# Kernel optimization log

Hardware: AMD Instinct MI355X
Metric: run time of the kernel (lower is better)

Reference implementation:

```python
import jax, jax.numpy as jnp
import numpy as np

B = 32768          # batch rows
IN_DIM = 512
HID = 64           # hidden_dim fixed in module
COMM = 128         # output_dim == proto_latent_dim (num_simultaneous_tokens=1)
P = 2048           # num_protos
BETA = 0.25        # settings.alpha != 0
KL_W = 1.0         # settings.kl_weight
ENT_W = 0.1        # settings.entropy_weight
EPSILON = 1e-8


def setup_inputs() -> dict:
    key = jax.random.key(0)
    ks = jax.random.split(key, 16)
    s = 0.05
    return {
        "x": jax.random.normal(ks[0], (B, IN_DIM), jnp.float32),
        "eps": jax.random.normal(ks[1], (B, COMM), jnp.float32),
        "W_emb": jax.random.normal(ks[2], (IN_DIM, HID), jnp.float32) * s,
        "b_emb": jnp.zeros((HID,), jnp.float32),
        "W1": jax.random.normal(ks[3], (HID, HID), jnp.float32) * s,
        "b1": jnp.zeros((HID,), jnp.float32),
        "W2": jax.random.normal(ks[4], (HID, COMM), jnp.float32) * s,
        "b2": jnp.zeros((COMM,), jnp.float32),
        "W_mu": jax.random.normal(ks[5], (COMM, COMM), jnp.float32) * s,
        "b_mu": jnp.zeros((COMM,), jnp.float32),
        "W_var": jax.random.normal(ks[6], (COMM, COMM), jnp.float32) * s,
        "b_var": jnp.zeros((COMM,), jnp.float32),
        "protos": jax.random.uniform(ks[7], (P, COMM), jnp.float32, -1.0 / P, 1.0 / P),
    }


def _sq_dists(a, b):
    # ||a||^2 + ||b||^2 - 2 a b^T  -> [N, P] without [N,P,D] intermediate
    return (jnp.sum(a * a, axis=1, keepdims=True)
            + jnp.sum(b * b, axis=1)
            - 2.0 * a @ b.T)


def reference(x, eps, W_emb, b_emb, W1, b1, W2, b2, W_mu, b_mu, W_var, b_var, protos):
    sg = jax.lax.stop_gradient
    h = x @ W_emb + b_emb                       # [B, HID]
    h = h.reshape(-1, HID)                      # num_imgs = 1
    h = jax.nn.relu(h @ W1 + b1)
    h = jax.nn.relu(h @ W2 + b2)                # [B, COMM]
    r = h.reshape(-1, COMM)
    mu = r @ W_mu + b_mu
    logvar = r @ W_var + b_var
    sample = mu + jnp.exp(0.5 * logvar) * eps   # reparameterize

    # VQ: pairwise squared dists, argmin routing, codebook gather
    dists = _sq_dists(sample, protos)           # [B, P]
    idx = jnp.argmin(dists, axis=1)             # [B]
    quantized = protos[idx]                     # [B, COMM]

    commitment_loss = jnp.mean((sg(quantized) - mu) ** 2)
    embedding_loss = jnp.mean((quantized - sg(mu)) ** 2)
    vq_loss = BETA * commitment_loss + embedding_loss

    # entropy term: softmax-like row probs from Gaussian kernel on mu-proto dists
    # sum(((mu-p)/2)^2, -1) == ||mu-p||^2 / 4, computed via matmul form
    neg_dist = -0.5 * (_sq_dists(mu, protos) / 4.0)
    exponents = jnp.exp(neg_dist) + EPSILON     # [B, P]
    row_probs = exponents / jnp.sum(exponents, axis=1, keepdims=True)
    approx_probs = jnp.mean(row_probs, axis=0)  # [P]
    ent = jnp.sum(-approx_probs * jnp.log(approx_probs))
    vq_loss = vq_loss + ENT_W * ent

    # straight-through estimator
    q_st = sample + sg(quantized - sample)
    output = q_st.reshape(-1, COMM)

    kld = jnp.mean(-0.5 * jnp.sum(1.0 + logvar - mu ** 2 - jnp.exp(logvar), axis=1))
    total_loss = KL_W * kld + vq_loss
    return output, total_loss, kld
```

## Files before the change

kernel.cpp:

```cpp
#include <hip/hip_runtime.h>
#include <cmath>

constexpr int NB   = 32768;
constexpr int IND  = 512;
constexpr int HIDD = 64;
constexpr int CM   = 128;
constexpr int NP   = 2048;
constexpr float BETA  = 0.25f;
constexpr float ENT_W = 0.1f;
constexpr float EPSV  = 1e-8f;

typedef __attribute__((ext_vector_type(8))) short short8v;
typedef __attribute__((ext_vector_type(4))) float f32x4v;

__device__ __forceinline__ float4 ld4(const float* p){ return *reinterpret_cast<const float4*>(p); }
__device__ __forceinline__ void  st4(float* p, float4 v){ *reinterpret_cast<float4*>(p) = v; }

__device__ __forceinline__ unsigned short f2bf(float f){
  union { float f; unsigned u; } v; v.f = f;
  unsigned r = v.u + 0x7fffu + ((v.u >> 16) & 1u);
  return (unsigned short)(r >> 16);
}
__device__ __forceinline__ float bf2f(unsigned short u){
  union { unsigned u; float f; } v; v.u = ((unsigned)u) << 16;
  return v.f;
}
__device__ __forceinline__ short8v cvt8(float4 a, float4 b){
  short8v r;
  r[0]=(short)f2bf(a.x); r[1]=(short)f2bf(a.y); r[2]=(short)f2bf(a.z); r[3]=(short)f2bf(a.w);
  r[4]=(short)f2bf(b.x); r[5]=(short)f2bf(b.y); r[6]=(short)f2bf(b.z); r[7]=(short)f2bf(b.w);
  return r;
}

__device__ __forceinline__ float wave_sum(float v){
  #pragma unroll
  for (int m = 1; m < 64; m <<= 1) v += __shfl_xor(v, m, 64);
  return v;
}

typedef __attribute__((address_space(1))) unsigned int gu32;
typedef __attribute__((address_space(3))) unsigned int su32;
__device__ __forceinline__ void gload_lds16(const void* g, void* s){
  __builtin_amdgcn_global_load_lds((const gu32*)g, (su32*)s, 16, 0, 0);
}
__device__ __forceinline__ void gload_lds4(const void* g, void* s){
  __builtin_amdgcn_global_load_lds((const gu32*)g, (su32*)s, 4, 0, 0);
}
__device__ __forceinline__ void barrier_raw(){
  __builtin_amdgcn_sched_barrier(0);
  __builtin_amdgcn_s_barrier();
  __builtin_amdgcn_sched_barrier(0);
}

__global__ __launch_bounds__(256) void k_prep(const float* __restrict__ protos,
                                              float* __restrict__ normp2,
                                              unsigned short* __restrict__ pBF,
                                              const float* __restrict__ W_emb,
                                              const float* __restrict__ W1,
                                              const float* __restrict__ W2,
                                              const float* __restrict__ Wmu,
                                              const float* __restrict__ Wvar,
                                              unsigned short* __restrict__ WembT,
                                              unsigned short* __restrict__ W1T,
                                              unsigned short* __restrict__ W2T,
                                              unsigned short* __restrict__ WmuT,
                                              unsigned short* __restrict__ WvarT){
  const int b = blockIdx.x, tid = threadIdx.x;
  if (b < 8){
    const int p = b * 256 + tid;
    const float* row = protos + (size_t)p * CM;
    float s = 0.f;
    #pragma unroll
    for (int k = 0; k < CM; k += 4){
      float4 v = ld4(row + k);
      s += v.x*v.x + v.y*v.y + v.z*v.z + v.w*v.w;
      ushort4 u; u.x = f2bf(v.x); u.y = f2bf(v.y); u.z = f2bf(v.z); u.w = f2bf(v.w);
      *reinterpret_cast<ushort4*>(&pBF[(size_t)p * CM + k]) = u;
    }
    normp2[p] = s;
  } else if (b < 16){
    const int nb = (b - 8) * 8;
    for (int i = tid; i < 8*512; i += 256){
      const int n = nb + (i >> 9), k = i & 511;
      WembT[n*512 + k] = f2bf(W_emb[k*64 + n]);
    }
  } else if (b == 16){
    for (int i = tid; i < 64*64; i += 256){
      const int n = i >> 6, k = i & 63;
      W1T[n*64 + k] = f2bf(W1[k*64 + n]);
    }
  } else if (b == 17){
    for (int i = tid; i < 128*64; i += 256){
      const int n = i >> 6, k = i & 63;
      W2T[n*64 + k] = f2bf(W2[k*128 + n]);
    }
  } else if (b < 20){
    const int nb = (b - 18) * 64;
    for (int i = tid; i < 64*128; i += 256){
      const int n = nb + (i >> 7), k = i & 127;
      WmuT[n*128 + k] = f2bf(Wmu[k*128 + n]);
    }
  } else {
    const int nb = (b - 20) * 64;
    for (int i = tid; i < 64*128; i += 256){
      const int n = nb + (i >> 7), k = i & 127;
      WvarT[n*128 + k] = f2bf(Wvar[k*128 + n]);
    }
  }
}

__global__ __launch_bounds__(256, 4) void fwd_fused(const float* __restrict__ x,
    const unsigned short* __restrict__ WembT, const float* __restrict__ b_emb,
    const unsigned short* __restrict__ W1T,   const float* __restrict__ b1,
    const unsigned short* __restrict__ W2T,   const float* __restrict__ b2,
    const unsigned short* __restrict__ WmuT,  const float* __restrict__ bmu,
    const unsigned short* __restrict__ WvarT, const float* __restrict__ bvar,
    const float* __restrict__ epsIn,
    unsigned short* __restrict__ muBF, unsigned short* __restrict__ sBF,
    float* __restrict__ normMu2, float* __restrict__ kld_part){
  __shared__ __align__(16) unsigned short SH[16384];
  __shared__ __align__(16) unsigned short Xs[4096];
  unsigned short* h1s = SH;
  unsigned short* h2s = SH + 4096;
  unsigned short* h3s = SH + 8192;
  unsigned short* muS = SH;
  unsigned short* sS  = SH + 8192;
  __shared__ float redbuf[4];

  const int tid = threadIdx.x;
  const int w = tid >> 6, l = tid & 63;
  const int lr = l >> 4, lc = l & 15;
  const int rowbase = blockIdx.x * 64;
  const int row = w*16 + lc;

  f32x4v acc1[4];
  #pragma unroll
  for (int nt = 0; nt < 4; nt++) acc1[nt] = (f32x4v){0.f,0.f,0.f,0.f};
  const int srow = tid >> 2, sq = tid & 3;
  const float* xrow = x + (size_t)(rowbase + srow) * IND + sq*16;
  for (int kc8 = 0; kc8 < 8; kc8++){
    float4 v0 = ld4(xrow + kc8*64);
    float4 v1 = ld4(xrow + kc8*64 + 4);
    float4 v2 = ld4(xrow + kc8*64 + 8);
    float4 v3 = ld4(xrow + kc8*64 + 12);
    __syncthreads();
    const int b0 = (srow*64 + sq*16)     ^ ((srow & 7) << 3);
    const int b1i = (srow*64 + sq*16 + 8) ^ ((srow & 7) << 3);
    *reinterpret_cast<short8v*>(&Xs[b0])  = cvt8(v0, v1);
    *reinterpret_cast<short8v*>(&Xs[b1i]) = cvt8(v2, v3);
    __syncthreads();
    #pragma unroll
    for (int ks = 0; ks < 2; ks++){
      const int ai = (row*64 + ks*32 + lr*8) ^ ((row & 7) << 3);
      short8v af = *reinterpret_cast<const short8v*>(&Xs[ai]);
      #pragma unroll
      for (int nt = 0; nt < 4; nt++){
        const int n = nt*16 + lc;
        short8v bf = *reinterpret_cast<const short8v*>(&WembT[(size_t)n*512 + kc8*64 + ks*32 + lr*8]);
        acc1[nt] = __builtin_amdgcn_mfma_f32_16x16x32_bf16(af, bf, acc1[nt], 0, 0, 0);
      }
    }
  }
  #pragma unroll
  for (int nt = 0; nt < 4; nt++){
    const int col = nt*16 + lc;
    const float bb = b_emb[col];
    #pragma unroll
    for (int r = 0; r < 4; r++){
      const int row2 = w*16 + lr*4 + r;
      h1s[(row2*64 + col) ^ ((row2 & 7) << 3)] = f2bf(acc1[nt][r] + bb);
    }
  }
  __syncthreads();

  f32x4v acc2[4];
  #pragma unroll
  for (int nt = 0; nt < 4; nt++) acc2[nt] = (f32x4v){0.f,0.f,0.f,0.f};
  #pragma unroll
  for (int ks = 0; ks < 2; ks++){
    const int ai = (row*64 + ks*32 + lr*8) ^ ((row & 7) << 3);
    short8v af = *reinterpret_cast<const short8v*>(&h1s[ai]);
    #pragma unroll
    for (int nt = 0; nt < 4; nt++){
      const int n = nt*16 + lc;
      short8v bf = *reinterpret_cast<const short8v*>(&W1T[(size_t)n*64 + ks*32 + lr*8]);
      acc2[nt] = __builtin_amdgcn_mfma_f32_16x16x32_bf16(af, bf, acc2[nt], 0, 0, 0);
    }
  }
  __syncthreads();
  #pragma unroll
  for (int nt = 0; nt < 4; nt++){
    const int col = nt*16 + lc;
    const float bb = b1[col];
    #pragma unroll
    for (int r = 0; r < 4; r++){
      const int row2 = w*16 + lr*4 + r;
      h2s[(row2*64 + col) ^ ((row2 & 7) << 3)] = f2bf(fmaxf(acc2[nt][r] + bb, 0.f));
    }
  }
  __syncthreads();

  f32x4v acc3[8];
  #pragma unroll
  for (int nt = 0; nt < 8; nt++) acc3[nt] = (f32x4v){0.f,0.f,0.f,0.f};
  #pragma unroll
  for (int ks = 0; ks < 2; ks++){
    const int ai = (row*64 + ks*32 + lr*8) ^ ((row & 7) << 3);
    short8v af = *reinterpret_cast<const short8v*>(&h2s[ai]);
    #pragma unroll
    for (int nt = 0; nt < 8; nt++){
      const int n = nt*16 + lc;
      short8v bf = *reinterpret_cast<const short8v*>(&W2T[(size_t)n*64 + ks*32 + lr*8]);
      acc3[nt] = __builtin_amdgcn_mfma_f32_16x16x32_bf16(af, bf, acc3[nt], 0, 0, 0);
    }
  }
  #pragma unroll
  for (int nt = 0; nt < 8; nt++){
    const int col = nt*16 + lc;
    const float bb = b2[col];
    #pragma unroll
    for (int r = 0; r < 4; r++){
      const int row2 = w*16 + lr*4 + r;
      h3s[(row2*128 + col) ^ ((row2 & 7) << 3)] = f2bf(fmaxf(acc3[nt][r] + bb, 0.f));
    }
  }
  __syncthreads();

  f32x4v accM[8], accV[8];
  #pragma unroll
  for (int nt = 0; nt < 8; nt++){ accM[nt] = (f32x4v){0.f,0.f,0.f,0.f}; accV[nt] = (f32x4v){0.f,0.f,0.f,0.f}; }
  #pragma unroll
  for (int ks = 0; ks < 4; ks++){
    const int ai = (row*128 + ks*32 + lr*8) ^ ((row & 7) << 3);
    short8v af = *reinterpret_cast<const short8v*>(&h3s[ai]);
    #pragma unroll
    for (int nt = 0; nt < 8; nt++){
      const int n = nt*16 + lc;
      short8v bM = *reinterpret_cast<const short8v*>(&WmuT [(size_t)n*128 + ks*32 + lr*8]);
      short8v bV = *reinterpret_cast<const short8v*>(&WvarT[(size_t)n*128 + ks*32 + lr*8]);
      accM[nt] = __builtin_amdgcn_mfma_f32_16x16x32_bf16(af, bM, accM[nt], 0, 0, 0);
      accV[nt] = __builtin_amdgcn_mfma_f32_16x16x32_bf16(af, bV, accV[nt], 0, 0, 0);
    }
  }
  __syncthreads();

  float kl = 0.f;
  float m2[4] = {0.f, 0.f, 0.f, 0.f};
  #pragma unroll
  for (int nt = 0; nt < 8; nt++){
    const int col = nt*16 + lc;
    const float bm = bmu[col], bv = bvar[col];
    #pragma unroll
    for (int r = 0; r < 4; r++){
      const int row2 = w*16 + lr*4 + r;
      const float mu = accM[nt][r] + bm;
      const float lv = accV[nt][r] + bv;
      const float s2 = __expf(0.5f * lv);
      const float sa = mu + s2 * epsIn[(size_t)(rowbase + row2)*CM + col];
      kl += 1.f + lv - mu*mu - s2*s2;
      m2[r] += mu*mu;
      const int li = (row2*128 + col) ^ ((row2 & 7) << 3);
      muS[li] = f2bf(mu);
      sS [li] = f2bf(sa);
    }
  }
  #pragma unroll
  for (int m = 1; m < 16; m <<= 1){
    #pragma unroll
    for (int r = 0; r < 4; r++) m2[r] += __shfl_xor(m2[r], m, 64);
  }
  if (lc == 0){
    #pragma unroll
    for (int r = 0; r < 4; r++) normMu2[rowbase + w*16 + lr*4 + r] = m2[r];
  }
  const float kw = wave_sum(kl);
  if (l == 0) redbuf[w] = kw;
  __syncthreads();
  if (tid == 0) kld_part[blockIdx.x] = redbuf[0]+redbuf[1]+redbuf[2]+redbuf[3];
  {
    const int r2 = tid >> 2, kq = tid & 3;
    #pragma unroll
    for (int i = 0; i < 4; i++){
      const int k = kq*32 + i*8;
      const int li = (r2*128 + k) ^ ((r2 & 7) << 3);
      short8v vm = *reinterpret_cast<const short8v*>(&muS[li]);
      short8v vs = *reinterpret_cast<const short8v*>(&sS[li]);
      *reinterpret_cast<short8v*>(&muBF[(size_t)(rowbase + r2)*CM + k]) = vm;
      *reinterpret_cast<short8v*>(&sBF [(size_t)(rowbase + r2)*CM + k]) = vs;
    }
  }
}

__global__ __launch_bounds__(512, 4) void proto_merged(
    const unsigned short* __restrict__ sBF, const unsigned short* __restrict__ mBF,
    const unsigned short* __restrict__ pBF, const float* __restrict__ normp2,
    const float* __restrict__ normMu2, const float* __restrict__ protosF,
    float* __restrict__ outA, float* __restrict__ approx_part,
    float* __restrict__ commit_part)
{
  __shared__ __align__(16) unsigned short Ps[3][64*CM];
  __shared__ float Pn[3][64];
  __shared__ float approxl[NP];
  __shared__ float bw[2][64];
  __shared__ int   iw[2][64];
  __shared__ float sw[2][64];
  __shared__ float srow_s[64];
  __shared__ int   bidx_s[64];
  __shared__ float redbuf[8];

  const int tid = threadIdx.x;
  const int w = tid >> 6, l = tid & 63;
  const int lr = l >> 4, lc = l & 15;
  const int rw = w & 1;
  const int pw = (w >> 1) & 1;
  const int mat = w >> 2;
  const int rowbase = blockIdx.x * 64;

  for (int t = tid; t < NP; t += 512) approxl[t] = 0.f;

  const unsigned short* Abase = mat ? mBF : sBF;
  short8v af[2][4];
  #pragma unroll
  for (int mt = 0; mt < 2; mt++){
    const size_t rg = (size_t)(rowbase + rw*32 + mt*16 + lc) * CM;
    #pragma unroll
    for (int ks = 0; ks < 4; ks++)
      af[mt][ks] = *reinterpret_cast<const short8v*>(&Abase[rg + ks*32 + lr*8]);
  }
  float nmn[8];
  #pragma unroll
  for (int mt = 0; mt < 2; mt++)
    #pragma unroll
    for (int r = 0; r < 4; r++)
      nmn[mt*4+r] = -0.125f * normMu2[rowbase + rw*32 + mt*16 + lr*4 + r];

  #define STAGE(pc, buf) {                                                        \
    _Pragma("unroll")                                                             \
    for (int j = 0; j < 2; j++){                                                  \
      const int p = w*8 + j*4 + (l >> 4);                                         \
      const int g = l & 15;                                                       \
      gload_lds16(&pBF[(size_t)((pc) + p)*CM + ((g*8) ^ ((p & 7)*8))],            \
                  &Ps[buf][(w*8 + j*4)*CM]);                                      \
    }                                                                             \
    if (w == 0) gload_lds4(&normp2[(pc) + l], &Pn[buf][0]);                       \
  }
  #define VWAIT_PEND() { if (w == 0) asm volatile("s_waitcnt vmcnt(3)" ::: "memory"); \
                         else        asm volatile("s_waitcnt vmcnt(2)" ::: "memory"); }
  #define VWAIT_ALL()  asm volatile("s_waitcnt vmcnt(0)" ::: "memory")

  float best[8]; int bidx[8]; float sr[8];
  #pragma unroll
  for (int i = 0; i < 8; i++){ best[i] = 3.4e38f; bidx[i] = 0; sr[i] = 0.f; }

  STAGE(0, 0);
  int cur = 0;
  for (int c = 0; c < 32; c++){
    const int nxt = (cur == 2) ? 0 : cur + 1;
    if (c < 31){ STAGE((c+1)*64, nxt); VWAIT_PEND(); }
    else       { VWAIT_ALL(); }
    barrier_raw();
    const float npv0 = Pn[cur][pw*32 + lc];
    const float npv1 = Pn[cur][pw*32 + 16 + lc];
    f32x4v acc[2][2];
    #pragma unroll
    for (int mt = 0; mt < 2; mt++)
      #pragma unroll
      for (int nt = 0; nt < 2; nt++) acc[mt][nt] = (f32x4v){0.f,0.f,0.f,0.f};
    #pragma unroll
    for (int ks = 0; ks < 4; ks++){
      const int pl0 = pw*32 + lc;
      const int pl1 = pw*32 + 16 + lc;
      short8v pf0 = *reinterpret_cast<const short8v*>(&Ps[cur][(pl0*CM + ks*32 + lr*8) ^ ((pl0 & 7) << 3)]);
      short8v pf1 = *reinterpret_cast<const short8v*>(&Ps[cur][(pl1*CM + ks*32 + lr*8) ^ ((pl1 & 7) << 3)]);
      #pragma unroll
      for (int mt = 0; mt < 2; mt++){
        acc[mt][0] = __builtin_amdgcn_mfma_f32_16x16x32_bf16(af[mt][ks], pf0, acc[mt][0], 0, 0, 0);
        acc[mt][1] = __builtin_amdgcn_mfma_f32_16x16x32_bf16(af[mt][ks], pf1, acc[mt][1], 0, 0, 0);
      }
    }
    const int pc = c*64;
    if (mat == 0){
      #pragma unroll
      for (int nt = 0; nt < 2; nt++){
        const int pg = pc + pw*32 + nt*16 + lc;
        const float npv = nt ? npv1 : npv0;
        #pragma unroll
        for (int mt = 0; mt < 2; mt++)
          #pragma unroll
          for (int r = 0; r < 4; r++){
            const float sc = fmaf(-2.f, acc[mt][nt][r], npv);
            if (sc < best[mt*4+r]){ best[mt*4+r] = sc; bidx[mt*4+r] = pg; }
          }
      }
    } else {
      #pragma unroll
      for (int nt = 0; nt < 2; nt++){
        const float pvn = -0.125f * (nt ? npv1 : npv0);
        #pragma unroll
        for (int mt = 0; mt < 2; mt++)
          #pragma unroll
          for (int r = 0; r < 4; r++)
            sr[mt*4+r] += __expf(fmaf(0.25f, acc[mt][nt][r], nmn[mt*4+r] + pvn));
      }
    }
    cur = nxt;
  }

  if (mat == 0){
    #pragma unroll
    for (int m = 1; m < 16; m <<= 1){
      #pragma unroll
      for (int i = 0; i < 8; i++){
        const float ob = __shfl_xor(best[i], m, 64);
        const int   oi = __shfl_xor(bidx[i], m, 64);
        if (ob < best[i] || (ob == best[i] && oi < bidx[i])){ best[i] = ob; bidx[i] = oi; }
      }
    }
    if (lc == 0){
      #pragma unroll
      for (int mt = 0; mt < 2; mt++)
        #pragma unroll
        for (int r = 0; r < 4; r++){
          const int row = rw*32 + mt*16 + lr*4 + r;
          bw[pw][row] = best[mt*4+r];
          iw[pw][row] = bidx[mt*4+r];
        }
    }
  } else {
    #pragma unroll
    for (int m = 1; m < 16; m <<= 1){
      #pragma unroll
      for (int i = 0; i < 8; i++) sr[i] += __shfl_xor(sr[i], m, 64);
    }
    if (lc == 0){
      #pragma unroll
      for (int mt = 0; mt < 2; mt++)
        #pragma unroll
        for (int r = 0; r < 4; r++){
          const int row = rw*32 + mt*16 + lr*4 + r;
          sw[pw][row] = sr[mt*4+r];
        }
    }
  }
  __syncthreads();
  if (tid < 64){
    float b0 = bw[0][tid]; int i0 = iw[0][tid];
    const float b1 = bw[1][tid]; const int i1 = iw[1][tid];
    if (b1 < b0 || (b1 == b0 && i1 < i0)){ b0 = b1; i0 = i1; }
    bidx_s[tid] = i0;
    srow_s[tid] = sw[0][tid] + sw[1][tid] + (float)NP * EPSV;
  }
  STAGE(0, 0);
  __syncthreads();

  {
    const int row = tid >> 3, cp = tid & 7;
    const int rowg = rowbase + row;
    const int idx = bidx_s[row];
    float cl = 0.f;
    #pragma unroll
    for (int c4 = 0; c4 < 4; c4++){
      const int cc = c4*32 + cp*4;
      float4 q = ld4(protosF + (size_t)idx * CM + cc);
      ushort4 mb = *reinterpret_cast<const ushort4*>(&mBF[(size_t)rowg * CM + cc]);
      st4(outA + (size_t)rowg * CM + cc, q);
      const float dx=q.x-bf2f(mb.x), dy=q.y-bf2f(mb.y), dz=q.z-bf2f(mb.z), dw=q.w-bf2f(mb.w);
      cl += dx*dx + dy*dy + dz*dz + dw*dw;
    }
    const float cw = wave_sum(cl);
    if (l == 0) redbuf[w] = cw;
  }
  float rs[8]; float epsc = 0.f;
  #pragma unroll
  for (int mt = 0; mt < 2; mt++)
    #pragma unroll
    for (int r = 0; r < 4; r++){
      rs[mt*4+r] = 1.0f / srow_s[rw*32 + mt*16 + lr*4 + r];
      epsc += rs[mt*4+r];
    }
  epsc *= EPSV;
  if (mat == 0){
    #pragma unroll
    for (int mt = 0; mt < 2; mt++){
      const size_t rg = (size_t)(rowbase + rw*32 + mt*16 + lc) * CM;
      #pragma unroll
      for (int ks = 0; ks < 4; ks++)
        af[mt][ks] = *reinterpret_cast<const short8v*>(&mBF[rg + ks*32 + lr*8]);
    }
  }
  __syncthreads();
  if (tid == 0) commit_part[blockIdx.x] = redbuf[0]+redbuf[1]+redbuf[2]+redbuf[3]
                                        + redbuf[4]+redbuf[5]+redbuf[6]+redbuf[7];

  const int pq = w >> 1;
  cur = 0;
  for (int c = 0; c < 32; c++){
    const int nxt = (cur == 2) ? 0 : cur + 1;
    if (c < 31){ STAGE((c+1)*64, nxt); VWAIT_PEND(); }
    else       { VWAIT_ALL(); }
    barrier_raw();
    const int pl = pq*16 + lc;
    const float npv = Pn[cur][pl];
    f32x4v accB[2];
    accB[0] = (f32x4v){0.f,0.f,0.f,0.f};
    accB[1] = (f32x4v){0.f,0.f,0.f,0.f};
    #pragma unroll
    for (int ks = 0; ks < 4; ks++){
      short8v pf = *reinterpret_cast<const short8v*>(&Ps[cur][(pl*CM + ks*32 + lr*8) ^ ((pl & 7) << 3)]);
      accB[0] = __builtin_amdgcn_mfma_f32_16x16x32_bf16(af[0][ks], pf, accB[0], 0, 0, 0);
      accB[1] = __builtin_amdgcn_mfma_f32_16x16x32_bf16(af[1][ks], pf, accB[1], 0, 0, 0);
    }
    const float pvn = -0.125f * npv;
    float cs = epsc;
    #pragma unroll
    for (int mt = 0; mt < 2; mt++)
      #pragma unroll
      for (int r = 0; r < 4; r++){
        const float e = __expf(fmaf(0.25f, accB[mt][r], nmn[mt*4+r] + pvn));
        cs = fmaf(e, rs[mt*4+r], cs);
      }
    cs += __shfl_xor(cs, 16, 64);
    cs += __shfl_xor(cs, 32, 64);
    if (l < 16) atomicAdd(&approxl[c*64 + pq*16 + lc], cs);
    cur = nxt;
  }
  __syncthreads();
  for (int t = tid; t < NP; t += 512)
    approx_part[(size_t)blockIdx.x * NP + t] = approxl[t];
  #undef STAGE
  #undef VWAIT_PEND
  #undef VWAIT_ALL
}

__global__ __launch_bounds__(256) void k4a(const float* __restrict__ approx_part,
                                           float* __restrict__ ent_part){
  __shared__ float red[128];
  const int tid = threadIdx.x;
  const int p = blockIdx.x * 32 + (tid & 31);
  const int slice = tid >> 5;
  float s = 0.f;
  for (int b = slice; b < 512; b += 8) s += approx_part[(size_t)b * NP + p];
  s += __shfl_xor(s, 32, 64);
  if ((tid & 63) < 32) red[(tid >> 6)*32 + (tid & 31)] = s;
  __syncthreads();
  if (tid < 32){
    const float a = (red[tid] + red[32+tid] + red[64+tid] + red[96+tid]) * (1.0f / 32768.0f);
    float t = -a * logf(a);
    #pragma unroll
    for (int m = 1; m < 32; m <<= 1) t += __shfl_xor(t, m, 32);
    if (tid == 0) ent_part[blockIdx.x] = t;
  }
}

__global__ __launch_bounds__(256) void k4b(const float* __restrict__ kld_part,
                                           const float* __restrict__ commit_part,
                                           const float* __restrict__ ent_part,
                                           float* __restrict__ outs){
  __shared__ float redbuf[8];
  const int tid = threadIdx.x;
  float k = 0.f, c = 0.f;
  for (int i = tid; i < 512; i += 256){ k += kld_part[i]; c += commit_part[i]; }
  float kw = wave_sum(k), cw = wave_sum(c);
  if ((tid & 63) == 0){ redbuf[tid >> 6] = kw; redbuf[4 + (tid >> 6)] = cw; }
  __syncthreads();
  if (tid == 0){
    float ks = redbuf[0] + redbuf[1] + redbuf[2] + redbuf[3];
    float cs = redbuf[4] + redbuf[5] + redbuf[6] + redbuf[7];
    float es = 0.f;
    for (int i = 0; i < 64; i++) es += ent_part[i];
    float kld = -0.5f * ks / 32768.0f;
    float m = cs / (32768.0f * 128.0f);
    float vq = BETA * m + m + ENT_W * es;
    outs[0] = kld + vq;
    outs[1] = kld;
  }
}

extern "C" void kernel_launch(void* const* d_in, const int* in_sizes, int n_in,
                              void* d_out, int out_size, void* d_ws, size_t ws_size,
                              hipStream_t stream){
  const float* x      = (const float*)d_in[0];
  const float* epsIn  = (const float*)d_in[1];
  const float* W_emb  = (const float*)d_in[2];
  const float* b_emb  = (const float*)d_in[3];
  const float* W1     = (const float*)d_in[4];
  const float* b1     = (const float*)d_in[5];
  const float* W2     = (const float*)d_in[6];
  const float* b2     = (const float*)d_in[7];
  const float* W_mu   = (const float*)d_in[8];
  const float* b_mu   = (const float*)d_in[9];
  const float* W_var  = (const float*)d_in[10];
  const float* b_var  = (const float*)d_in[11];
  const float* protos = (const float*)d_in[12];
  float* out = (float*)d_out;
  float* ws = (float*)d_ws;

  const size_t M1 = 1024u * 1024u;
  unsigned short* mBF  = (unsigned short*)ws;
  unsigned short* sBF  = (unsigned short*)(ws + 2*M1);
  float* approx_part = ws + 4*M1;
  float* tail = ws + 5*M1;
  float* normMu2     = tail;
  float* normp2      = normMu2 + 32768;
  float* kld_part    = normp2 + 2048;
  float* commit_part = kld_part + 512;
  float* ent_part    = commit_part + 512;
  unsigned short* pBF   = (unsigned short*)(ent_part + 64);
  unsigned short* WembT = pBF + (size_t)NP*CM;
  unsigned short* W1T   = WembT + 64*512;
  unsigned short* W2T   = W1T + 64*64;
  unsigned short* WmuT  = W2T + 128*64;
  unsigned short* WvarT = WmuT + 128*128;

  k_prep<<<22, 256, 0, stream>>>(protos, normp2, pBF, W_emb, W1, W2, W_mu, W_var,
                                 WembT, W1T, W2T, WmuT, WvarT);
  fwd_fused<<<NB/64, 256, 0, stream>>>(x, WembT, b_emb, W1T, b1, W2T, b2,
                                       WmuT, b_mu, WvarT, b_var, epsIn,
                                       mBF, sBF, normMu2, kld_part);
  proto_merged<<<NB/64, 512, 0, stream>>>(sBF, mBF, pBF, normp2, normMu2,
                                          protos, out, approx_part, commit_part);
  k4a<<<64, 256, 0, stream>>>(approx_part, ent_part);
  k4b<<<1, 256, 0, stream>>>(kld_part, commit_part, ent_part, out + (size_t)NB * CM);
}
```

Baseline: 165.7 us.

## Fuse MLP encoder kernel into proto distance kernel, keep mu/sample in LDS

Merges the encoder MLP kernel and the prototype distance/argmin/entropy kernel into a single 512-thread kernel. mu and sample stay in shared memory as bf16 instead of round-tripping through global memory, and the first prototype tile is staged before the KL epilogue so its load overlaps that work. The MLP work is now split across 8 waves, each covering half the output columns. LDS is repartitioned into one aliased buffer, which raises shared-memory use per block and may reduce occupancy.

```diff
diff --git a/kernel.cpp b/kernel.cpp
--- a/kernel.cpp
+++ b/kernel.cpp
@@ -109,198 +109,21 @@
   }
 }
 
-__global__ __launch_bounds__(256, 4) void fwd_fused(const float* __restrict__ x,
+__global__ __launch_bounds__(512, 4) void mega(const float* __restrict__ x,
     const unsigned short* __restrict__ WembT, const float* __restrict__ b_emb,
     const unsigned short* __restrict__ W1T,   const float* __restrict__ b1,
     const unsigned short* __restrict__ W2T,   const float* __restrict__ b2,
     const unsigned short* __restrict__ WmuT,  const float* __restrict__ bmu,
     const unsigned short* __restrict__ WvarT, const float* __restrict__ bvar,
     const float* __restrict__ epsIn,
-    unsigned short* __restrict__ muBF, unsigned short* __restrict__ sBF,
-    float* __restrict__ normMu2, float* __restrict__ kld_part){
-  __shared__ __align__(16) unsigned short SH[16384];
-  __shared__ __align__(16) unsigned short Xs[4096];
-  unsigned short* h1s = SH;
-  unsigned short* h2s = SH + 4096;
-  unsigned short* h3s = SH + 8192;
-  unsigned short* muS = SH;
-  unsigned short* sS  = SH + 8192;
-  __shared__ float redbuf[4];
-
-  const int tid = threadIdx.x;
-  const int w = tid >> 6, l = tid & 63;
-  const int lr = l >> 4, lc = l & 15;
-  const int rowbase = blockIdx.x * 64;
-  const int row = w*16 + lc;
-
-  f32x4v acc1[4];
-  #pragma unroll
-  for (int nt = 0; nt < 4; nt++) acc1[nt] = (f32x4v){0.f,0.f,0.f,0.f};
-  const int srow = tid >> 2, sq = tid & 3;
-  const float* xrow = x + (size_t)(rowbase + srow) * IND + sq*16;
-  for (int kc8 = 0; kc8 < 8; kc8++){
-    float4 v0 = ld4(xrow + kc8*64);
-    float4 v1 = ld4(xrow + kc8*64 + 4);
-    float4 v2 = ld4(xrow + kc8*64 + 8);
-    float4 v3 = ld4(xrow + kc8*64 + 12);
-    __syncthreads();
-    const int b0 = (srow*64 + sq*16)     ^ ((srow & 7) << 3);
-    const int b1i = (srow*64 + sq*16 + 8) ^ ((srow & 7) << 3);
-    *reinterpret_cast<short8v*>(&Xs[b0])  = cvt8(v0, v1);
-    *reinterpret_cast<short8v*>(&Xs[b1i]) = cvt8(v2, v3);
-    __syncthreads();
-    #pragma unroll
-    for (int ks = 0; ks < 2; ks++){
-      const int ai = (row*64 + ks*32 + lr*8) ^ ((row & 7) << 3);
-      short8v af = *reinterpret_cast<const short8v*>(&Xs[ai]);
-      #pragma unroll
-      for (int nt = 0; nt < 4; nt++){
-        const int n = nt*16 + lc;
-        short8v bf = *reinterpret_cast<const short8v*>(&WembT[(size_t)n*512 + kc8*64 + ks*32 + lr*8]);
-        acc1[nt] = __builtin_amdgcn_mfma_f32_16x16x32_bf16(af, bf, acc1[nt], 0, 0, 0);
-      }
-    }
-  }
-  #pragma unroll
-  for (int nt = 0; nt < 4; nt++){
-    const int col = nt*16 + lc;
-    const float bb = b_emb[col];
-    #pragma unroll
-    for (int r = 0; r < 4; r++){
-      const int row2 = w*16 + lr*4 + r;
-      h1s[(row2*64 + col) ^ ((row2 & 7) << 3)] = f2bf(acc1[nt][r] + bb);
-    }
-  }
-  __syncthreads();
-
-  f32x4v acc2[4];
-  #pragma unroll
-  for (int nt = 0; nt < 4; nt++) acc2[nt] = (f32x4v){0.f,0.f,0.f,0.f};
-  #pragma unroll
-  for (int ks = 0; ks < 2; ks++){
-    const int ai = (row*64 + ks*32 + lr*8) ^ ((row & 7) << 3);
-    short8v af = *reinterpret_cast<const short8v*>(&h1s[ai]);
-    #pragma unroll
-    for (int nt = 0; nt < 4; nt++){
-      const int n = nt*16 + lc;
-      short8v bf = *reinterpret_cast<const short8v*>(&W1T[(size_t)n*64 + ks*32 + lr*8]);
-      acc2[nt] = __builtin_amdgcn_mfma_f32_16x16x32_bf16(af, bf, acc2[nt], 0, 0, 0);
-    }
-  }
-  __syncthreads();
-  #pragma unroll
-  for (int nt = 0; nt < 4; nt++){
-    const int col = nt*16 + lc;
-    const float bb = b1[col];
-    #pragma unroll
-    for (int r = 0; r < 4; r++){
-      const int row2 = w*16 + lr*4 + r;
-      h2s[(row2*64 + col) ^ ((row2 & 7) << 3)] = f2bf(fmaxf(acc2[nt][r] + bb, 0.f));
-    }
-  }
-  __syncthreads();
-
-  f32x4v acc3[8];
-  #pragma unroll
-  for (int nt = 0; nt < 8; nt++) acc3[nt] = (f32x4v){0.f,0.f,0.f,0.f};
-  #pragma unroll
-  for (int ks = 0; ks < 2; ks++){
-    const int ai = (row*64 + ks*32 + lr*8) ^ ((row & 7) << 3);
-    short8v af = *reinterpret_cast<const short8v*>(&h2s[ai]);
-    #pragma unroll
-    for (int nt = 0; nt < 8; nt++){
-      const int n = nt*16 + lc;
-      short8v bf = *reinterpret_cast<const short8v*>(&W2T[(size_t)n*64 + ks*32 + lr*8]);
-      acc3[nt] = __builtin_amdgcn_mfma_f32_16x16x32_bf16(af, bf, acc3[nt], 0, 0, 0);
-    }
-  }
-  #pragma unroll
-  for (int nt = 0; nt < 8; nt++){
-    const int col = nt*16 + lc;
-    const float bb = b2[col];
-    #pragma unroll
-    for (int r = 0; r < 4; r++){
-      const int row2 = w*16 + lr*4 + r;
-      h3s[(row2*128 + col) ^ ((row2 & 7) << 3)] = f2bf(fmaxf(acc3[nt][r] + bb, 0.f));
-    }
-  }
-  __syncthreads();
-
-  f32x4v accM[8], accV[8];
-  #pragma unroll
-  for (int nt = 0; nt < 8; nt++){ accM[nt] = (f32x4v){0.f,0.f,0.f,0.f}; accV[nt] = (f32x4v){0.f,0.f,0.f,0.f}; }
-  #pragma unroll
-  for (int ks = 0; ks < 4; ks++){
-    const int ai = (row*128 + ks*32 + lr*8) ^ ((row & 7) << 3);
-    short8v af = *reinterpret_cast<const short8v*>(&h3s[ai]);
-    #pragma unroll
-    for (int nt = 0; nt < 8; nt++){
-      const int n = nt*16 + lc;
-      short8v bM = *reinterpret_cast<const short8v*>(&WmuT [(size_t)n*128 + ks*32 + lr*8]);
-      short8v bV = *reinterpret_cast<const short8v*>(&WvarT[(size_t)n*128 + ks*32 + lr*8]);
-      accM[nt] = __builtin_amdgcn_mfma_f32_16x16x32_bf16(af, bM, accM[nt], 0, 0, 0);
-      accV[nt] = __builtin_amdgcn_mfma_f32_16x16x32_bf16(af, bV, accV[nt], 0, 0, 0);
-    }
-  }
-  __syncthreads();
-
-  float kl = 0.f;
-  float m2[4] = {0.f, 0.f, 0.f, 0.f};
-  #pragma unroll
-  for (int nt = 0; nt < 8; nt++){
-    const int col = nt*16 + lc;
-    const float bm = bmu[col], bv = bvar[col];
-    #pragma unroll
-    for (int r = 0; r < 4; r++){
-      const int row2 = w*16 + lr*4 + r;
-      const float mu = accM[nt][r] + bm;
-      const float lv = accV[nt][r] + bv;
-      const float s2 = __expf(0.5f * lv);
-      const float sa = mu + s2 * epsIn[(size_t)(rowbase + row2)*CM + col];
-      kl += 1.f + lv - mu*mu - s2*s2;
-      m2[r] += mu*mu;
-      const int li = (row2*128 + col) ^ ((row2 & 7) << 3);
-      muS[li] = f2bf(mu);
-      sS [li] = f2bf(sa);
-    }
-  }
-  #pragma unroll
-  for (int m = 1; m < 16; m <<= 1){
-    #pragma unroll
-    for (int r = 0; r < 4; r++) m2[r] += __shfl_xor(m2[r], m, 64);
-  }
-  if (lc == 0){
-    #pragma unroll
-    for (int r = 0; r < 4; r++) normMu2[rowbase + w*16 + lr*4 + r] = m2[r];
-  }
-  const float kw = wave_sum(kl);
-  if (l == 0) redbuf[w] = kw;
-  __syncthreads();
-  if (tid == 0) kld_part[blockIdx.x] = redbuf[0]+redbuf[1]+redbuf[2]+redbuf[3];
-  {
-    const int r2 = tid >> 2, kq = tid & 3;
-    #pragma unroll
-    for (int i = 0; i < 4; i++){
-      const int k = kq*32 + i*8;
-      const int li = (r2*128 + k) ^ ((r2 & 7) << 3);
-      short8v vm = *reinterpret_cast<const short8v*>(&muS[li]);
-      short8v vs = *reinterpret_cast<const short8v*>(&sS[li]);
-      *reinterpret_cast<short8v*>(&muBF[(size_t)(rowbase + r2)*CM + k]) = vm;
-      *reinterpret_cast<short8v*>(&sBF [(size_t)(rowbase + r2)*CM + k]) = vs;
-    }
-  }
-}
-
-__global__ __launch_bounds__(512, 4) void proto_merged(
-    const unsigned short* __restrict__ sBF, const unsigned short* __restrict__ mBF,
     const unsigned short* __restrict__ pBF, const float* __restrict__ normp2,
-    const float* __restrict__ normMu2, const float* __restrict__ protosF,
+    const float* __restrict__ protosF,
     float* __restrict__ outA, float* __restrict__ approx_part,
-    float* __restrict__ commit_part)
+    float* __restrict__ commit_part, float* __restrict__ kld_part)
 {
-  __shared__ __align__(16) unsigned short Ps[3][64*CM];
+  __shared__ __align__(16) unsigned short SH[36864];
   __shared__ float Pn[3][64];
-  __shared__ float approxl[NP];
+  __shared__ float nm2_s[2][64];
   __shared__ float bw[2][64];
   __shared__ int   iw[2][64];
   __shared__ float sw[2][64];
@@ -308,31 +131,128 @@
   __shared__ int   bidx_s[64];
   __shared__ float redbuf[8];
 
+  unsigned short* muS = SH;
+  float* approxl      = (float*)(SH + 8192);
+  unsigned short* PsU = SH + 12288;
+  unsigned short* Xs  = PsU;
+  unsigned short* h1s = PsU + 4096;
+  unsigned short* h2s = PsU + 8192;
+  unsigned short* h3s = PsU + 12288;
+  unsigned short* sS  = PsU + 16384;
+
   const int tid = threadIdx.x;
   const int w = tid >> 6, l = tid & 63;
   const int lr = l >> 4, lc = l & 15;
-  const int rw = w & 1;
-  const int pw = (w >> 1) & 1;
-  const int mat = w >> 2;
   const int rowbase = blockIdx.x * 64;
 
-  for (int t = tid; t < NP; t += 512) approxl[t] = 0.f;
-
-  const unsigned short* Abase = mat ? mBF : sBF;
-  short8v af[2][4];
-  #pragma unroll
-  for (int mt = 0; mt < 2; mt++){
-    const size_t rg = (size_t)(rowbase + rw*32 + mt*16 + lc) * CM;
-    #pragma unroll
-    for (int ks = 0; ks < 4; ks++)
-      af[mt][ks] = *reinterpret_cast<const short8v*>(&Abase[rg + ks*32 + lr*8]);
-  }
-  float nmn[8];
-  #pragma unroll
-  for (int mt = 0; mt < 2; mt++)
-    #pragma unroll
-    for (int r = 0; r < 4; r++)
-      nmn[mt*4+r] = -0.125f * normMu2[rowbase + rw*32 + mt*16 + lr*4 + r];
+  const int rq = w & 3, nh = w >> 2;
+  const int row = rq*16 + lc;
+
+  f32x4v acc1[2];
+  acc1[0] = (f32x4v){0.f,0.f,0.f,0.f}; acc1[1] = (f32x4v){0.f,0.f,0.f,0.f};
+  const int srow = tid >> 3, sq = tid & 7;
+  const float* xrow = x + (size_t)(rowbase + srow) * IND + sq*8;
+  for (int kc8 = 0; kc8 < 8; kc8++){
+    float4 v0 = ld4(xrow + kc8*64);
+    float4 v1 = ld4(xrow + kc8*64 + 4);
+    __syncthreads();
+    *reinterpret_cast<short8v*>(&Xs[(srow*64 + sq*8) ^ ((srow & 7) << 3)]) = cvt8(v0, v1);
+    __syncthreads();
+    #pragma unroll
+    for (int ks = 0; ks < 2; ks++){
+      const int ai = (row*64 + ks*32 + lr*8) ^ ((row & 7) << 3);
+      short8v af = *reinterpret_cast<const short8v*>(&Xs[ai]);
+      #pragma unroll
+      for (int nt = 0; nt < 2; nt++){
+        const int n = nh*32 + nt*16 + lc;
+        short8v bf = *reinterpret_cast<const short8v*>(&WembT[(size_t)n*512 + kc8*64 + ks*32 + lr*8]);
+        acc1[nt] = __builtin_amdgcn_mfma_f32_16x16x32_bf16(af, bf, acc1[nt], 0, 0, 0);
+      }
+    }
+  }
+  __syncthreads();
+  #pragma unroll
+  for (int nt = 0; nt < 2; nt++){
+    const int col = nh*32 + nt*16 + lc;
+    const float bb = b_emb[col];
+    #pragma unroll
+    for (int r = 0; r < 4; r++){
+      const int row2 = rq*16 + lr*4 + r;
+      h1s[(row2*64 + col) ^ ((row2 & 7) << 3)] = f2bf(acc1[nt][r] + bb);
+    }
+  }
+  __syncthreads();
+
+  f32x4v acc2[2];
+  acc2[0] = (f32x4v){0.f,0.f,0.f,0.f}; acc2[1] = (f32x4v){0.f,0.f,0.f,0.f};
+  #pragma unroll
+  for (int ks = 0; ks < 2; ks++){
+    const int ai = (row*64 + ks*32 + lr*8) ^ ((row & 7) << 3);
+    short8v af = *reinterpret_cast<const short8v*>(&h1s[ai]);
+    #pragma unroll
+    for (int nt = 0; nt < 2; nt++){
+      const int n = nh*32 + nt*16 + lc;
+      short8v bf = *reinterpret_cast<const short8v*>(&W1T[(size_t)n*64 + ks*32 + lr*8]);
+      acc2[nt] = __builtin_amdgcn_mfma_f32_16x16x32_bf16(af, bf, acc2[nt], 0, 0, 0);
+    }
+  }
+  __syncthreads();
+  #pragma unroll
+  for (int nt = 0; nt < 2; nt++){
+    const int col = nh*32 + nt*16 + lc;
+    const float bb = b1[col];
+    #pragma unroll
+    for (int r = 0; r < 4; r++){
+      const int row2 = rq*16 + lr*4 + r;
+      h2s[(row2*64 + col) ^ ((row2 & 7) << 3)] = f2bf(fmaxf(acc2[nt][r] + bb, 0.f));
+    }
+  }
+  __syncthreads();
+
+  f32x4v acc3[4];
+  #pragma unroll
+  for (int nt = 0; nt < 4; nt++) acc3[nt] = (f32x4v){0.f,0.f,0.f,0.f};
+  #pragma unroll
+  for (int ks = 0; ks < 2; ks++){
+    const int ai = (row*64 + ks*32 + lr*8) ^ ((row & 7) << 3);
+    short8v af = *reinterpret_cast<const short8v*>(&h2s[ai]);
+    #pragma unroll
+    for (int nt = 0; nt < 4; nt++){
+      const int n = nh*64 + nt*16 + lc;
+      short8v bf = *reinterpret_cast<const short8v*>(&W2T[(size_t)n*64 + ks*32 + lr*8]);
+      acc3[nt] = __builtin_amdgcn_mfma_f32_16x16x32_bf16(af, bf, acc3[nt], 0, 0, 0);
+    }
+  }
+  __syncthreads();
+  #pragma unroll
+  for (int nt = 0; nt < 4; nt++){
+    const int col = nh*64 + nt*16 + lc;
+    const float bb = b2[col];
+    #pragma unroll
+    for (int r = 0; r < 4; r++){
+      const int row2 = rq*16 + lr*4 + r;
+      h3s[(row2*128 + col) ^ ((row2 & 7) << 3)] = f2bf(fmaxf(acc3[nt][r] + bb, 0.f));
+    }
+  }
+  __syncthreads();
+
+  f32x4v accM[4], accV[4];
+  #pragma unroll
+  for (int nt = 0; nt < 4; nt++){ accM[nt] = (f32x4v){0.f,0.f,0.f,0.f}; accV[nt] = (f32x4v){0.f,0.f,0.f,0.f}; }
+  #pragma unroll
+  for (int ks = 0; ks < 4; ks++){
+    const int ai = (row*128 + ks*32 + lr*8) ^ ((row & 7) << 3);
+    short8v af = *reinterpret_cast<const short8v*>(&h3s[ai]);
+    #pragma unroll
+    for (int nt = 0; nt < 4; nt++){
+      const int n = nh*64 + nt*16 + lc;
+      short8v bM = *reinterpret_cast<const short8v*>(&WmuT [(size_t)n*128 + ks*32 + lr*8]);
+      short8v bV = *reinterpret_cast<const short8v*>(&WvarT[(size_t)n*128 + ks*32 + lr*8]);
+      accM[nt] = __builtin_amdgcn_mfma_f32_16x16x32_bf16(af, bM, accM[nt], 0, 0, 0);
+      accV[nt] = __builtin_amdgcn_mfma_f32_16x16x32_bf16(af, bV, accV[nt], 0, 0, 0);
+    }
+  }
+  __syncthreads();
 
   #define STAGE(pc, buf) {                                                        \
     _Pragma("unroll")                                                             \
@@ -340,7 +260,7 @@
       const int p = w*8 + j*4 + (l >> 4);                                         \
       const int g = l & 15;                                                       \
       gload_lds16(&pBF[(size_t)((pc) + p)*CM + ((g*8) ^ ((p & 7)*8))],            \
-                  &Ps[buf][(w*8 + j*4)*CM]);                                      \
+                  &PsU[(size_t)(buf)*8192 + (w*8 + j*4)*CM]);                     \
     }                                                                             \
     if (w == 0) gload_lds4(&normp2[(pc) + l], &Pn[buf][0]);                       \
   }
@@ -348,11 +268,73 @@
                          else        asm volatile("s_waitcnt vmcnt(2)" ::: "memory"); }
   #define VWAIT_ALL()  asm volatile("s_waitcnt vmcnt(0)" ::: "memory")
 
+  STAGE(0, 0);
+
+  {
+    float kl = 0.f;
+    float m2[4] = {0.f, 0.f, 0.f, 0.f};
+    #pragma unroll
+    for (int nt = 0; nt < 4; nt++){
+      const int col = nh*64 + nt*16 + lc;
+      const float bm = bmu[col], bv = bvar[col];
+      #pragma unroll
+      for (int r = 0; r < 4; r++){
+        const int row2 = rq*16 + lr*4 + r;
+        const float mu = accM[nt][r] + bm;
+        const float lv = accV[nt][r] + bv;
+        const float s2 = __expf(0.5f * lv);
+        const float sa = mu + s2 * epsIn[(size_t)(rowbase + row2)*CM + col];
+        kl += 1.f + lv - mu*mu - s2*s2;
+        m2[r] += mu*mu;
+        const int li = (row2*128 + col) ^ ((row2 & 7) << 3);
+        muS[li] = f2bf(mu);
+        sS [li] = f2bf(sa);
+      }
+    }
+    #pragma unroll
+    for (int m = 1; m < 16; m <<= 1){
+      #pragma unroll
+      for (int r = 0; r < 4; r++) m2[r] += __shfl_xor(m2[r], m, 64);
+    }
+    if (lc == 0){
+      #pragma unroll
+      for (int r = 0; r < 4; r++) nm2_s[nh][rq*16 + lr*4 + r] = m2[r];
+    }
+    const float kw = wave_sum(kl);
+    if (l == 0) redbuf[w] = kw;
+  }
+  __syncthreads();
+  if (tid == 0) kld_part[blockIdx.x] = redbuf[0]+redbuf[1]+redbuf[2]+redbuf[3]
+                                     + redbuf[4]+redbuf[5]+redbuf[6]+redbuf[7];
+
+  const int rw = w & 1;
+  const int pw = (w >> 1) & 1;
+  const int mat = w >> 2;
+
+  const unsigned short* Abase = mat ? muS : sS;
+  short8v af[2][4];
+  #pragma unroll
+  for (int mt = 0; mt < 2; mt++){
+    const int ar = rw*32 + mt*16 + lc;
+    #pragma unroll
+    for (int ks = 0; ks < 4; ks++)
+      af[mt][ks] = *reinterpret_cast<const short8v*>(&Abase[(ar*128 + ks*32 + lr*8) ^ ((ar & 7) << 3)]);
+  }
+  float nmn[8];
+  #pragma unroll
+  for (int mt = 0; mt < 2; mt++)
+    #pragma unroll
+    for (int r = 0; r < 4; r++){
+      const int rr = rw*32 + mt*16 + lr*4 + r;
+      nmn[mt*4+r] = -0.125f * (nm2_s[0][rr] + nm2_s[1][rr]);
+    }
+  __syncthreads();
+  for (int t = tid; t < NP; t += 512) approxl[t] = 0.f;
+
   float best[8]; int bidx[8]; float sr[8];
   #pragma unroll
   for (int i = 0; i < 8; i++){ best[i] = 3.4e38f; bidx[i] = 0; sr[i] = 0.f; }
 
-  STAGE(0, 0);
   int cur = 0;
   for (int c = 0; c < 32; c++){
     const int nxt = (cur == 2) ? 0 : cur + 1;
@@ -361,6 +343,7 @@
     barrier_raw();
     const float npv0 = Pn[cur][pw*32 + lc];
     const float npv1 = Pn[cur][pw*32 + 16 + lc];
+    const unsigned short* pb = &PsU[(size_t)cur*8192];
     f32x4v acc[2][2];
     #pragma unroll
     for (int mt = 0; mt < 2; mt++)
@@ -370,8 +353,8 @@
     for (int ks = 0; ks < 4; ks++){
       const int pl0 = pw*32 + lc;
       const int pl1 = pw*32 + 16 + lc;
-      short8v pf0 = *reinterpret_cast<const short8v*>(&Ps[cur][(pl0*CM + ks*32 + lr*8) ^ ((pl0 & 7) << 3)]);
-      short8v pf1 = *reinterpret_cast<const short8v*>(&Ps[cur][(pl1*CM + ks*32 + lr*8) ^ ((pl1 & 7) << 3)]);
+      short8v pf0 = *reinterpret_cast<const short8v*>(&pb[(pl0*CM + ks*32 + lr*8) ^ ((pl0 & 7) << 3)]);
+      short8v pf1 = *reinterpret_cast<const short8v*>(&pb[(pl1*CM + ks*32 + lr*8) ^ ((pl1 & 7) << 3)]);
       #pragma unroll
       for (int mt = 0; mt < 2; mt++){
         acc[mt][0] = __builtin_amdgcn_mfma_f32_16x16x32_bf16(af[mt][ks], pf0, acc[mt][0], 0, 0, 0);
@@ -421,9 +404,9 @@
       for (int mt = 0; mt < 2; mt++)
         #pragma unroll
         for (int r = 0; r < 4; r++){
-          const int row = rw*32 + mt*16 + lr*4 + r;
-          bw[pw][row] = best[mt*4+r];
-          iw[pw][row] = bidx[mt*4+r];
+          const int rr = rw*32 + mt*16 + lr*4 + r;
+          bw[pw][rr] = best[mt*4+r];
+          iw[pw][rr] = bidx[mt*4+r];
         }
     }
   } else {
@@ -437,8 +420,8 @@
       for (int mt = 0; mt < 2; mt++)
         #pragma unroll
         for (int r = 0; r < 4; r++){
-          const int row = rw*32 + mt*16 + lr*4 + r;
-          sw[pw][row] = sr[mt*4+r];
+          const int rr = rw*32 + mt*16 + lr*4 + r;
+          sw[pw][rr] = sr[mt*4+r];
         }
     }
   }
@@ -454,15 +437,16 @@
   __syncthreads();
 
   {
-    const int row = tid >> 3, cp = tid & 7;
-    const int rowg = rowbase + row;
-    const int idx = bidx_s[row];
+    const int orow = tid >> 3, cp = tid & 7;
+    const int rowg = rowbase + orow;
+    const int idx = bidx_s[orow];
     float cl = 0.f;
     #pragma unroll
     for (int c4 = 0; c4 < 4; c4++){
       const int cc = c4*32 + cp*4;
       float4 q = ld4(protosF + (size_t)idx * CM + cc);
-      ushort4 mb = *reinterpret_cast<const ushort4*>(&mBF[(size_t)rowg * CM + cc]);
+      const int li = (orow*128 + cc) ^ ((orow & 7) << 3);
+      ushort4 mb = *reinterpret_cast<const ushort4*>(&muS[li]);
       st4(outA + (size_t)rowg * CM + cc, q);
       const float dx=q.x-bf2f(mb.x), dy=q.y-bf2f(mb.y), dz=q.z-bf2f(mb.z), dw=q.w-bf2f(mb.w);
       cl += dx*dx + dy*dy + dz*dz + dw*dw;
@@ -482,10 +466,10 @@
   if (mat == 0){
     #pragma unroll
     for (int mt = 0; mt < 2; mt++){
-      const size_t rg = (size_t)(rowbase + rw*32 + mt*16 + lc) * CM;
+      const int ar = rw*32 + mt*16 + lc;
       #pragma unroll
       for (int ks = 0; ks < 4; ks++)
-        af[mt][ks] = *reinterpret_cast<const short8v*>(&mBF[rg + ks*32 + lr*8]);
+        af[mt][ks] = *reinterpret_cast<const short8v*>(&muS[(ar*128 + ks*32 + lr*8) ^ ((ar & 7) << 3)]);
     }
   }
   __syncthreads();
@@ -501,12 +485,13 @@
     barrier_raw();
     const int pl = pq*16 + lc;
     const float npv = Pn[cur][pl];
+    const unsigned short* pb = &PsU[(size_t)cur*8192];
     f32x4v accB[2];
     accB[0] = (f32x4v){0.f,0.f,0.f,0.f};
     accB[1] = (f32x4v){0.f,0.f,0.f,0.f};
     #pragma unroll
     for (int ks = 0; ks < 4; ks++){
-      short8v pf = *reinterpret_cast<const short8v*>(&Ps[cur][(pl*CM + ks*32 + lr*8) ^ ((pl & 7) << 3)]);
+      short8v pf = *reinterpret_cast<const short8v*>(&pb[(pl*CM + ks*32 + lr*8) ^ ((pl & 7) << 3)]);
       accB[0] = __builtin_amdgcn_mfma_f32_16x16x32_bf16(af[0][ks], pf, accB[0], 0, 0, 0);
       accB[1] = __builtin_amdgcn_mfma_f32_16x16x32_bf16(af[1][ks], pf, accB[1], 0, 0, 0);
     }
@@ -596,12 +581,9 @@
   float* ws = (float*)d_ws;
 
   const size_t M1 = 1024u * 1024u;
-  unsigned short* mBF  = (unsigned short*)ws;
-  unsigned short* sBF  = (unsigned short*)(ws + 2*M1);
-  float* approx_part = ws + 4*M1;
-  float* tail = ws + 5*M1;
-  float* normMu2     = tail;
-  float* normp2      = normMu2 + 32768;
+  float* approx_part = ws;
+  float* tail = ws + M1;
+  float* normp2      = tail;
   float* kld_part    = normp2 + 2048;
   float* commit_part = kld_part + 512;
   float* ent_part    = commit_part + 512;
@@ -614,11 +596,10 @@
 
   k_prep<<<22, 256, 0, stream>>>(protos, normp2, pBF, W_emb, W1, W2, W_mu, W_var,
                                  WembT, W1T, W2T, WmuT, WvarT);
-  fwd_fused<<<NB/64, 256, 0, stream>>>(x, WembT, b_emb, W1T, b1, W2T, b2,
-                                       WmuT, b_mu, WvarT, b_var, epsIn,
-                                       mBF, sBF, normMu2, kld_part);
-  proto_merged<<<NB/64, 512, 0, stream>>>(sBF, mBF, pBF, normp2, normMu2,
-                                          protos, out, approx_part, commit_part);
+  mega<<<NB/64, 512, 0, stream>>>(x, WembT, b_emb, W1T, b1, W2T, b2,
+                                  WmuT, b_mu, WvarT, b_var, epsIn,
+                                  pBF, normp2, protos,
+                                  out, approx_part, commit_part, kld_part);
   k4a<<<64, 256, 0, stream>>>(approx_part, ent_part);
   k4b<<<1, 256, 0, stream>>>(kld_part, commit_part, ent_part, out + (size_t)NB * CM);
 }
```

After: 155.0 us (median of 3 runs). -6.4%, faster.
